# Optimization experiments

Hardware: AMD Instinct MI355X
Metric: run time of the kernel (lower is better)

The kernel has to match this reference:

```python
import jax, jax.numpy as jnp
import numpy as np

B, H, W, C = 2, 64, 64, 256
NH, K = 8, 7  # num_heads, neighborhood kernel size


def setup_inputs() -> dict:
    key = jax.random.key(0)
    ks = jax.random.split(key, 8)
    xav = lambda k, shape: jax.random.normal(k, shape, jnp.float32) * np.sqrt(2.0 / (shape[0] + shape[1])).astype(np.float32)
    return {
        "x": jax.random.normal(ks[0], (B, H, W, C), jnp.float32),
        "norm1_g": jnp.ones((C,), jnp.float32),
        "norm1_b": jnp.zeros((C,), jnp.float32),
        "qkv_w": xav(ks[1], (3 * C, C)),
        "qkv_b": jnp.zeros((3 * C,), jnp.float32),
        "rpb": jax.random.normal(ks[2], (NH, 2 * K - 1, 2 * K - 1), jnp.float32) * 0.02,
        "proj_w": xav(ks[3], (C, C)),
        "proj_b": jnp.zeros((C,), jnp.float32),
        "norm2_g": jnp.ones((C,), jnp.float32),
        "norm2_b": jnp.zeros((C,), jnp.float32),
        "fc1_w": xav(ks[4], (4 * C, C)),
        "fc1_b": jnp.zeros((4 * C,), jnp.float32),
        "fc2_w": xav(ks[5], (C, 4 * C)),
        "fc2_b": jnp.zeros((C,), jnp.float32),
    }


def _layernorm(x, g, b, eps=1e-5):
    m = x.mean(-1, keepdims=True)
    v = jnp.mean((x - m) ** 2, axis=-1, keepdims=True)
    return (x - m) * jax.lax.rsqrt(v + eps) * g + b


def _nat2d(x, qkv_w, qkv_b, rpb, proj_w, proj_b):
    """Neighborhood attention 2D (NATTEN semantics: edge-clamped k x k windows,
    relative positional bias indexed by key_pos - query_pos + k - 1)."""
    b, h, w, c = x.shape
    nh = rpb.shape[0]
    k = (rpb.shape[1] + 1) // 2
    dh = c // nh
    qkv = (x @ qkv_w.T + qkv_b).reshape(b, h, w, 3, nh, dh)
    q = qkv[..., 0, :, :] * (dh ** -0.5)  # [b,h,w,nh,dh]
    kk = qkv[..., 1, :, :]
    vv = qkv[..., 2, :, :]
    # edge-clamped window starts per query row/col
    starts_h = jnp.clip(jnp.arange(h) - k // 2, 0, h - k)
    starts_w = jnp.clip(jnp.arange(w) - k // 2, 0, w - k)
    idx_h = starts_h[:, None] + jnp.arange(k)  # [h,k] key row indices
    idx_w = starts_w[:, None] + jnp.arange(k)  # [w,k] key col indices
    # gather neighborhoods -> [b,h,w,k,k,nh,dh]
    knb = kk[:, idx_h][:, :, :, idx_w].transpose(0, 1, 3, 2, 4, 5, 6)
    vnb = vv[:, idx_h][:, :, :, idx_w].transpose(0, 1, 3, 2, 4, 5, 6)
    attn = jnp.einsum('bijhd,bijklhd->bijhkl', q, knb)  # [b,h,w,nh,k,k]
    # relative positional bias: index = key - query + (k-1) in [0, 2k-2]
    rb_h = idx_h - jnp.arange(h)[:, None] + (k - 1)  # [h,k]
    rb_w = idx_w - jnp.arange(w)[:, None] + (k - 1)  # [w,k]
    bias = rpb[:, rb_h][:, :, :, rb_w]  # [nh,h,k,w,k]
    bias = bias.transpose(1, 3, 0, 2, 4)  # [h,w,nh,k,k]
    attn = jax.nn.softmax((attn + bias).reshape(b, h, w, nh, k * k), axis=-1)
    out = jnp.einsum('bijhn,bijnhd->bijhd', attn, vnb.reshape(b, h, w, k * k, nh, dh))
    return out.reshape(b, h, w, c) @ proj_w.T + proj_b


def reference(x, norm1_g, norm1_b, qkv_w, qkv_b, rpb, proj_w, proj_b,
              norm2_g, norm2_b, fc1_w, fc1_b, fc2_w, fc2_b):
    # norm -> neighborhood attention -> residual
    x = x + _nat2d(_layernorm(x, norm1_g, norm1_b), qkv_w, qkv_b, rpb, proj_w, proj_b)
    # norm -> MLP (gelu) -> residual
    hdn = _layernorm(x, norm2_g, norm2_b)
    hdn = jax.nn.gelu(hdn @ fc1_w.T + fc1_b, approximate=False)
    return x + (hdn @ fc2_w.T + fc2_b)
```

## Files before the change

kernel.cpp:

```cpp
#include <hip/hip_runtime.h>

typedef __attribute__((ext_vector_type(8))) short bf16x8;
typedef __attribute__((ext_vector_type(4))) float f32x4;
typedef unsigned short u16;

__device__ __forceinline__ float bf2f(u16 u) {
    return __builtin_bit_cast(float, ((unsigned int)u) << 16);
}
__device__ __forceinline__ u16 f2bf(float f) {
    unsigned int x = __builtin_bit_cast(unsigned int, f);
    x += 0x7FFFu + ((x >> 16) & 1u);
    return (u16)(x >> 16);
}

typedef const __attribute__((address_space(1))) void* gas_t;
typedef __attribute__((address_space(3))) void* las_t;
__device__ __forceinline__ void load_lds16(const u16* g, u16* l) {
    __builtin_amdgcn_global_load_lds((gas_t)g, (las_t)l, 16, 0, 0);
}

__global__ __launch_bounds__(256) void cvt_kernel(
    const float* __restrict__ s0, const float* __restrict__ s1,
    const float* __restrict__ s2, const float* __restrict__ s3,
    u16* __restrict__ dst)
{
    const int i4 = (blockIdx.x * 256 + threadIdx.x) * 4;
    const float* src;
    int off;
    if      (i4 < 196608) { src = s0; off = i4; }
    else if (i4 < 262144) { src = s1; off = i4 - 196608; }
    else if (i4 < 524288) { src = s2; off = i4 - 262144; }
    else                  { src = s3; off = i4 - 524288; }
    float4 v = *(const float4*)(src + off);
    ushort4 o;
    o.x = f2bf(v.x); o.y = f2bf(v.y); o.z = f2bf(v.z); o.w = f2bf(v.w);
    *(ushort4*)(dst + i4) = o;
}

__global__ __launch_bounds__(256) void ln_kernel(
    const float* __restrict__ x, const float* __restrict__ g,
    const float* __restrict__ b, u16* __restrict__ y)
{
    const int tok  = blockIdx.x * 4 + (threadIdx.x >> 6);
    const int lane = threadIdx.x & 63;
    float4 v = *(const float4*)(x + (size_t)tok * 256 + lane * 4);
    float s  = v.x + v.y + v.z + v.w;
    float sq = v.x*v.x + v.y*v.y + v.z*v.z + v.w*v.w;
    #pragma unroll
    for (int off = 32; off; off >>= 1) {
        s  += __shfl_xor(s, off);
        sq += __shfl_xor(sq, off);
    }
    float mean = s * (1.0f / 256.0f);
    float var  = sq * (1.0f / 256.0f) - mean * mean;
    float rs   = rsqrtf(var + 1e-5f);
    float4 gv = *(const float4*)(g + lane * 4);
    float4 bv = *(const float4*)(b + lane * 4);
    ushort4 o;
    o.x = f2bf((v.x - mean) * rs * gv.x + bv.x);
    o.y = f2bf((v.y - mean) * rs * gv.y + bv.y);
    o.z = f2bf((v.z - mean) * rs * gv.z + bv.z);
    o.w = f2bf((v.w - mean) * rs * gv.w + bv.w);
    *(ushort4*)(y + (size_t)tok * 256 + lane * 4) = o;
}

template<int N, int K, int EPI>
__global__ __launch_bounds__(256) void gemm64(
    const u16* __restrict__ A, const u16* __restrict__ W,
    const float* __restrict__ bias, const float* __restrict__ res,
    void* __restrict__ outv)
{
    __shared__ u16 As[64 * 64];
    __shared__ u16 Bs[64 * 64];
    const int tid  = threadIdx.x;
    const int lane = tid & 63;
    const int wave = tid >> 6;
    const int m0   = blockIdx.x * 64;
    const int n0   = blockIdx.y * 64;
    const int wm0  = (wave >> 1) * 32;
    const int wn0  = (wave & 1) * 32;

    f32x4 acc[2][2];
    #pragma unroll
    for (int mt = 0; mt < 2; ++mt)
        #pragma unroll
        for (int nt = 0; nt < 2; ++nt)
            acc[mt][nt] = (f32x4){0.f, 0.f, 0.f, 0.f};

    int soff[2];
    #pragma unroll
    for (int r = 0; r < 2; ++r) {
        const int s   = r * 256 + tid;
        const int row = s >> 3;
        const int c   = (s & 7) ^ (row & 7);
        soff[r] = row * K + c * 8;
    }
    const int fr = lane & 15;
    const int fc = lane >> 4;

    for (int k0 = 0; k0 < K; k0 += 64) {
        __syncthreads();
        #pragma unroll
        for (int r = 0; r < 2; ++r) {
            load_lds16(A + (size_t)m0 * K + k0 + soff[r], As + (r * 256 + tid) * 8);
            load_lds16(W + (size_t)n0 * K + k0 + soff[r], Bs + (r * 256 + tid) * 8);
        }
        __syncthreads();
        #pragma unroll
        for (int ks = 0; ks < 2; ++ks) {
            bf16x8 af[2], bw[2];
            #pragma unroll
            for (int mt = 0; mt < 2; ++mt) {
                const int rr   = wm0 + mt * 16 + fr;
                const int phys = (ks * 4 + fc) ^ (rr & 7);
                af[mt] = *(const bf16x8*)(As + rr * 64 + phys * 8);
            }
            #pragma unroll
            for (int nt = 0; nt < 2; ++nt) {
                const int rr   = wn0 + nt * 16 + fr;
                const int phys = (ks * 4 + fc) ^ (rr & 7);
                bw[nt] = *(const bf16x8*)(Bs + rr * 64 + phys * 8);
            }
            #pragma unroll
            for (int mt = 0; mt < 2; ++mt)
                #pragma unroll
                for (int nt = 0; nt < 2; ++nt)
                    acc[mt][nt] = __builtin_amdgcn_mfma_f32_16x16x32_bf16(af[mt], bw[nt], acc[mt][nt], 0, 0, 0);
        }
    }

    const int col = lane & 15;
    const int rb  = (lane >> 4) * 4;
    #pragma unroll
    for (int nt = 0; nt < 2; ++nt) {
        const int n  = n0 + wn0 + nt * 16 + col;
        const float bv = bias[n];
        #pragma unroll
        for (int mt = 0; mt < 2; ++mt) {
            #pragma unroll
            for (int r = 0; r < 4; ++r) {
                const int m = m0 + wm0 + mt * 16 + rb + r;
                float v = acc[mt][nt][r] + bv;
                if (EPI == 1) {
                    if (n < 256) v *= 0.1767766952966369f;
                    ((u16*)outv)[(size_t)m * N + n] = f2bf(v);
                }
                if (EPI == 2) {
                    v += res[(size_t)m * N + n];
                    ((float*)outv)[(size_t)m * N + n] = v;
                }
                if (EPI == 3) {
                    v = 0.5f * v * (1.0f + erff(v * 0.7071067811865475f));
                    ((u16*)outv)[(size_t)m * N + n] = f2bf(v);
                }
            }
        }
    }
}

__global__ __launch_bounds__(256, 2) void attn_tile_kernel(
    const u16* __restrict__ qkv, const float* __restrict__ rpb,
    u16* __restrict__ out)
{
    __shared__ u16   kv[100 * 64];
    __shared__ u16   qs[16 * 32];
    __shared__ float probs[16 * 66];

    const int tid  = threadIdx.x;
    const int bb   = blockIdx.x >> 8;
    const int rem  = blockIdx.x & 255;
    const int ti0  = (rem >> 4) << 2;
    const int tj0  = (rem & 15) << 2;
    const int oh   = min(max(ti0 - 3, 0), 54);
    const int ow   = min(max(tj0 - 3, 0), 54);
    const int tokbase = bb * 4096;

    int off_kv[4];
    #pragma unroll
    for (int r = 0; r < 4; ++r) {
        const int s  = r * 256 + tid;
        const int t  = s >> 3;
        const int cs = s & 7;
        const int c  = cs ^ (t & 7);
        const int tr = t / 10, tc = t - tr * 10;
        const int tokg = tokbase + (oh + tr) * 64 + (ow + tc);
        off_kv[r] = tokg * 768 + 256 + ((c & 4) << 6) + (c & 3) * 8;
    }
    const int tq   = tid >> 2;
    const int qoff = (tokbase + (ti0 + (tq >> 2)) * 64 + (tj0 + (tq & 3))) * 768
                   + (tid & 3) * 8;

    const int token = tid >> 4;
    const int part  = tid & 15;
    const int li = token >> 2, lj = token & 3;
    const int i  = ti0 + li,   j  = tj0 + lj;
    const int sh = min(max(i - 3, 0), 57);
    const int sw = min(max(j - 3, 0), 57);
    const int rowbase  = (sh - oh) * 10 + (sw - ow);
    const int rb_const = (sh - i + 6) * 13 + (sw - j + 6);
    const size_t outbase = (size_t)(tokbase + i * 64 + j) * 256 + part * 2;

    for (int h = 0; h < 8; ++h) {
        __syncthreads();
        const int hoff = h * 32;
        #pragma unroll
        for (int r = 0; r < 3; ++r)
            load_lds16(qkv + off_kv[r] + hoff, kv + (r * 256 + tid) * 8);
        if (tid < 32)
            load_lds16(qkv + off_kv[3] + hoff, kv + (768 + tid) * 8);
        if (tid < 64)
            load_lds16(qkv + qoff + hoff, qs + tid * 8);
        __syncthreads();

        float qv[32];
        #pragma unroll
        for (int c = 0; c < 4; ++c) {
            bf16x8 v = *(const bf16x8*)(qs + token * 32 + c * 8);
            #pragma unroll
            for (int e = 0; e < 8; ++e) qv[c * 8 + e] = bf2f((u16)v[e]);
        }

        float sc[4];
        #pragma unroll
        for (int sidx = 0; sidx < 4; ++sidx) {
            const int n = part + sidx * 16;
            if (n < 49) {
                const int kh = n / 7, kw = n - (n / 7) * 7;
                const int hidx = rowbase + kh * 10 + kw;
                float acc = rpb[h * 169 + rb_const + kh * 13 + kw];
                #pragma unroll
                for (int c = 0; c < 4; ++c) {
                    const int slot = (hidx << 3) + (c ^ (hidx & 7));
                    bf16x8 kk = *(const bf16x8*)(kv + slot * 8);
                    #pragma unroll
                    for (int e = 0; e < 8; ++e)
                        acc += qv[c * 8 + e] * bf2f((u16)kk[e]);
                }
                sc[sidx] = acc;
            } else {
                sc[sidx] = -1e30f;
            }
        }
        float mx = fmaxf(fmaxf(sc[0], sc[1]), fmaxf(sc[2], sc[3]));
        #pragma unroll
        for (int off = 1; off < 16; off <<= 1) mx = fmaxf(mx, __shfl_xor(mx, off));
        float ex[4], ssum = 0.f;
        #pragma unroll
        for (int sidx = 0; sidx < 4; ++sidx) {
            ex[sidx] = __expf(sc[sidx] - mx);
            ssum += ex[sidx];
        }
        #pragma unroll
        for (int off = 1; off < 16; off <<= 1) ssum += __shfl_xor(ssum, off);
        const float inv = 1.0f / ssum;
        #pragma unroll
        for (int sidx = 0; sidx < 4; ++sidx)
            probs[token * 66 + part + sidx * 16] = ex[sidx] * inv;
        __syncthreads();

        float o0 = 0.f, o1 = 0.f;
        const int vchunk = 4 + (part >> 2);
        const int vsub   = (part & 3) * 2;
        #pragma unroll
        for (int kh = 0; kh < 7; ++kh) {
            #pragma unroll
            for (int kw = 0; kw < 7; ++kw) {
                const int n    = kh * 7 + kw;
                const int hidx = rowbase + kh * 10 + kw;
                const float p  = probs[token * 66 + n];
                const int slot = (hidx << 3) + (vchunk ^ (hidx & 7));
                const unsigned int vv = *(const unsigned int*)(kv + slot * 8 + vsub);
                o0 += p * bf2f((u16)(vv & 0xffffu));
                o1 += p * bf2f((u16)(vv >> 16));
            }
        }
        ushort2 ov;
        ov.x = f2bf(o0); ov.y = f2bf(o1);
        *(ushort2*)(out + outbase + hoff) = ov;
    }
}

extern "C" void kernel_launch(void* const* d_in, const int* in_sizes, int n_in,
                              void* d_out, int out_size, void* d_ws, size_t ws_size,
                              hipStream_t stream)
{
    const float* x      = (const float*)d_in[0];
    const float* n1g    = (const float*)d_in[1];
    const float* n1b    = (const float*)d_in[2];
    const float* qkv_w  = (const float*)d_in[3];
    const float* qkv_b  = (const float*)d_in[4];
    const float* rpb    = (const float*)d_in[5];
    const float* proj_w = (const float*)d_in[6];
    const float* proj_b = (const float*)d_in[7];
    const float* n2g    = (const float*)d_in[8];
    const float* n2b    = (const float*)d_in[9];
    const float* fc1_w  = (const float*)d_in[10];
    const float* fc1_b  = (const float*)d_in[11];
    const float* fc2_w  = (const float*)d_in[12];
    const float* fc2_b  = (const float*)d_in[13];
    float* out = (float*)d_out;

    char* wsb = (char*)d_ws;
    u16*   wbf   = (u16*)wsb;
    u16*   qkvW  = wbf;
    u16*   projW = wbf + 196608;
    u16*   fc1W  = wbf + 262144;
    u16*   fc2W  = wbf + 524288;
    u16*   ln1   = (u16*)(wsb + 1572864);
    u16*   attn  = ln1;
    u16*   qkvB  = (u16*)(wsb + 5767168);
    u16*   ln2   = qkvB;
    u16*   hbuf  = (u16*)(wsb + 9961472);
    float* x1    = (float*)(wsb + 26738688);

    dim3 blk(256);
    cvt_kernel<<<768, blk, 0, stream>>>(qkv_w, proj_w, fc1_w, fc2_w, wbf);
    ln_kernel<<<2048, blk, 0, stream>>>(x, n1g, n1b, ln1);
    gemm64<768, 256, 1><<<dim3(128, 12), blk, 0, stream>>>(ln1, qkvW, qkv_b, nullptr, qkvB);
    attn_tile_kernel<<<512, blk, 0, stream>>>(qkvB, rpb, attn);
    gemm64<256, 256, 2><<<dim3(128, 4), blk, 0, stream>>>(attn, projW, proj_b, x, x1);
    ln_kernel<<<2048, blk, 0, stream>>>(x1, n2g, n2b, ln2);
    gemm64<1024, 256, 3><<<dim3(128, 16), blk, 0, stream>>>(ln2, fc1W, fc1_b, nullptr, hbuf);
    gemm64<256, 1024, 2><<<dim3(128, 4), blk, 0, stream>>>(hbuf, fc2W, fc2_b, x1, out);
}
```

Baseline: 165.1 us.

## Fuse whole block into persistent megakernel with grid barriers; fuse proj with LayerNorm2

```diff
diff --git a/kernel.cpp b/kernel.cpp
--- a/kernel.cpp
+++ b/kernel.cpp
@@ -3,6 +3,8 @@
 typedef __attribute__((ext_vector_type(8))) short bf16x8;
 typedef __attribute__((ext_vector_type(4))) float f32x4;
 typedef unsigned short u16;
+
+#define NBLK 512
 
 __device__ __forceinline__ float bf2f(u16 u) {
     return __builtin_bit_cast(float, ((unsigned int)u) << 16);
@@ -19,64 +21,33 @@
     __builtin_amdgcn_global_load_lds((gas_t)g, (las_t)l, 16, 0, 0);
 }
 
-__global__ __launch_bounds__(256) void cvt_kernel(
-    const float* __restrict__ s0, const float* __restrict__ s1,
-    const float* __restrict__ s2, const float* __restrict__ s3,
-    u16* __restrict__ dst)
+__global__ void init_bar(int* bar) {
+    if (threadIdx.x < 16) bar[threadIdx.x] = 0;
+}
+
+__device__ __forceinline__ void gridbar(int* bar, int idx) {
+    __syncthreads();
+    if (threadIdx.x == 0) {
+        __threadfence();
+        __hip_atomic_fetch_add(bar + idx, 1, __ATOMIC_ACQ_REL, __HIP_MEMORY_SCOPE_AGENT);
+        while (__hip_atomic_load(bar + idx, __ATOMIC_ACQUIRE, __HIP_MEMORY_SCOPE_AGENT) < NBLK)
+            __builtin_amdgcn_s_sleep(8);
+    }
+    __syncthreads();
+    __threadfence();
+}
+
+template<int N, int K, int EPI>
+__device__ void gemm_tile(int bx, int by, const u16* A, const u16* W,
+                          const float* bias, const float* res, void* outv, char* smem)
 {
-    const int i4 = (blockIdx.x * 256 + threadIdx.x) * 4;
-    const float* src;
-    int off;
-    if      (i4 < 196608) { src = s0; off = i4; }
-    else if (i4 < 262144) { src = s1; off = i4 - 196608; }
-    else if (i4 < 524288) { src = s2; off = i4 - 262144; }
-    else                  { src = s3; off = i4 - 524288; }
-    float4 v = *(const float4*)(src + off);
-    ushort4 o;
-    o.x = f2bf(v.x); o.y = f2bf(v.y); o.z = f2bf(v.z); o.w = f2bf(v.w);
-    *(ushort4*)(dst + i4) = o;
-}
-
-__global__ __launch_bounds__(256) void ln_kernel(
-    const float* __restrict__ x, const float* __restrict__ g,
-    const float* __restrict__ b, u16* __restrict__ y)
-{
-    const int tok  = blockIdx.x * 4 + (threadIdx.x >> 6);
-    const int lane = threadIdx.x & 63;
-    float4 v = *(const float4*)(x + (size_t)tok * 256 + lane * 4);
-    float s  = v.x + v.y + v.z + v.w;
-    float sq = v.x*v.x + v.y*v.y + v.z*v.z + v.w*v.w;
-    #pragma unroll
-    for (int off = 32; off; off >>= 1) {
-        s  += __shfl_xor(s, off);
-        sq += __shfl_xor(sq, off);
-    }
-    float mean = s * (1.0f / 256.0f);
-    float var  = sq * (1.0f / 256.0f) - mean * mean;
-    float rs   = rsqrtf(var + 1e-5f);
-    float4 gv = *(const float4*)(g + lane * 4);
-    float4 bv = *(const float4*)(b + lane * 4);
-    ushort4 o;
-    o.x = f2bf((v.x - mean) * rs * gv.x + bv.x);
-    o.y = f2bf((v.y - mean) * rs * gv.y + bv.y);
-    o.z = f2bf((v.z - mean) * rs * gv.z + bv.z);
-    o.w = f2bf((v.w - mean) * rs * gv.w + bv.w);
-    *(ushort4*)(y + (size_t)tok * 256 + lane * 4) = o;
-}
-
-template<int N, int K, int EPI>
-__global__ __launch_bounds__(256) void gemm64(
-    const u16* __restrict__ A, const u16* __restrict__ W,
-    const float* __restrict__ bias, const float* __restrict__ res,
-    void* __restrict__ outv)
-{
-    __shared__ u16 As[64 * 64];
-    __shared__ u16 Bs[64 * 64];
+    u16* As = (u16*)smem;
+    u16* Bs = (u16*)(smem + 8192);
     const int tid  = threadIdx.x;
     const int lane = tid & 63;
     const int wave = tid >> 6;
-    const int m0   = blockIdx.x * 64;
-    const int n0   = blockIdx.y * 64;
+    const int m0   = bx * 64;
+    const int n0   = by * 64;
     const int wm0  = (wave >> 1) * 32;
     const int wn0  = (wave & 1) * 32;
 
@@ -158,17 +129,106 @@
     }
 }
 
-__global__ __launch_bounds__(256, 2) void attn_tile_kernel(
-    const u16* __restrict__ qkv, const float* __restrict__ rpb,
-    u16* __restrict__ out)
+__device__ void proj_ln_tile(int bx, const u16* A, const u16* W, const float* pb,
+                             const float* xres, const float* g2, const float* b2,
+                             float* x1, u16* ln2out, char* smem)
 {
-    __shared__ u16   kv[100 * 64];
-    __shared__ u16   qs[16 * 32];
-    __shared__ float probs[16 * 66];
-
+    u16* As = (u16*)smem;
+    u16* Bs = (u16*)(smem + 4096);
     const int tid  = threadIdx.x;
-    const int bb   = blockIdx.x >> 8;
-    const int rem  = blockIdx.x & 255;
+    const int lane = tid & 63;
+    const int wave = tid >> 6;
+    const int m0   = bx * 64;
+
+    f32x4 acc[16];
+    #pragma unroll
+    for (int nt = 0; nt < 16; ++nt) acc[nt] = (f32x4){0.f, 0.f, 0.f, 0.f};
+
+    const int arow = tid >> 2, acs = tid & 3;
+    const int aoff = (m0 + arow) * 256 + (acs ^ (arow & 3)) * 8;
+    int boff[4];
+    #pragma unroll
+    for (int r = 0; r < 4; ++r) {
+        const int s   = r * 256 + tid;
+        const int row = s >> 2;
+        const int c   = (s & 3) ^ (row & 3);
+        boff[r] = row * 256 + c * 8;
+    }
+    const int fr = lane & 15;
+    const int fc = lane >> 4;
+
+    for (int k0 = 0; k0 < 256; k0 += 32) {
+        __syncthreads();
+        load_lds16(A + aoff + k0, As + tid * 8);
+        #pragma unroll
+        for (int r = 0; r < 4; ++r)
+            load_lds16(W + boff[r] + k0, Bs + (r * 256 + tid) * 8);
+        __syncthreads();
+        const int ra   = wave * 16 + fr;
+        const int pa   = fc ^ (ra & 3);
+        bf16x8 af = *(const bf16x8*)(As + ra * 32 + pa * 8);
+        #pragma unroll
+        for (int nt = 0; nt < 16; ++nt) {
+            const int rb_  = nt * 16 + fr;
+            const int pb_  = fc ^ (rb_ & 3);
+            bf16x8 bw = *(const bf16x8*)(Bs + rb_ * 32 + pb_ * 8);
+            acc[nt] = __builtin_amdgcn_mfma_f32_16x16x32_bf16(af, bw, acc[nt], 0, 0, 0);
+        }
+    }
+
+    const int col = lane & 15;
+    const int g   = lane >> 4;
+    float s[4] = {0.f, 0.f, 0.f, 0.f}, sq[4] = {0.f, 0.f, 0.f, 0.f};
+    #pragma unroll
+    for (int nt = 0; nt < 16; ++nt) {
+        const int n = nt * 16 + col;
+        const float bv = pb[n];
+        #pragma unroll
+        for (int r = 0; r < 4; ++r) {
+            const int m = m0 + wave * 16 + g * 4 + r;
+            float v = acc[nt][r] + bv + xres[(size_t)m * 256 + n];
+            acc[nt][r] = v;
+            s[r] += v; sq[r] += v * v;
+        }
+    }
+    #pragma unroll
+    for (int off = 1; off < 16; off <<= 1) {
+        #pragma unroll
+        for (int r = 0; r < 4; ++r) {
+            s[r]  += __shfl_xor(s[r], off);
+            sq[r] += __shfl_xor(sq[r], off);
+        }
+    }
+    float mean[4], rs[4];
+    #pragma unroll
+    for (int r = 0; r < 4; ++r) {
+        mean[r] = s[r] * (1.0f / 256.0f);
+        const float var = sq[r] * (1.0f / 256.0f) - mean[r] * mean[r];
+        rs[r] = rsqrtf(var + 1e-5f);
+    }
+    #pragma unroll
+    for (int nt = 0; nt < 16; ++nt) {
+        const int n = nt * 16 + col;
+        const float gam = g2[n], bet = b2[n];
+        #pragma unroll
+        for (int r = 0; r < 4; ++r) {
+            const int m = m0 + wave * 16 + g * 4 + r;
+            const float v = acc[nt][r];
+            x1[(size_t)m * 256 + n] = v;
+            ln2out[(size_t)m * 256 + n] = f2bf((v - mean[r]) * rs[r] * gam + bet);
+        }
+    }
+}
+
+__device__ void attn_tile(int bid, const u16* qkv, const float* rpb, u16* out, char* smem)
+{
+    u16*   kv    = (u16*)smem;
+    u16*   qs    = (u16*)(smem + 12800);
+    float* probs = (float*)(smem + 13824);
+
+    const int tid  = threadIdx.x;
+    const int bb   = bid >> 8;
+    const int rem  = bid & 255;
     const int ti0  = (rem >> 4) << 2;
     const int tj0  = (rem & 15) << 2;
     const int oh   = min(max(ti0 - 3, 0), 54);
@@ -178,10 +238,9 @@
     int off_kv[4];
     #pragma unroll
     for (int r = 0; r < 4; ++r) {
-        const int s  = r * 256 + tid;
-        const int t  = s >> 3;
-        const int cs = s & 7;
-        const int c  = cs ^ (t & 7);
+        const int sslot = r * 256 + tid;
+        const int t  = sslot >> 3;
+        const int c  = (sslot & 7) ^ (t & 7);
         const int tr = t / 10, tc = t - tr * 10;
         const int tokg = tokbase + (oh + tr) * 64 + (ow + tc);
         off_kv[r] = tokg * 768 + 256 + ((c & 4) << 6) + (c & 3) * 8;
@@ -278,6 +337,89 @@
         ov.x = f2bf(o0); ov.y = f2bf(o1);
         *(ushort2*)(out + outbase + hoff) = ov;
     }
+}
+
+__global__ __launch_bounds__(256, 2) void mega_kernel(
+    const float* __restrict__ x,
+    const float* __restrict__ n1g, const float* __restrict__ n1b,
+    const float* __restrict__ qkv_w, const float* __restrict__ qkv_b,
+    const float* __restrict__ rpb,
+    const float* __restrict__ proj_w, const float* __restrict__ proj_b,
+    const float* __restrict__ n2g, const float* __restrict__ n2b,
+    const float* __restrict__ fc1_w, const float* __restrict__ fc1_b,
+    const float* __restrict__ fc2_w, const float* __restrict__ fc2_b,
+    float* __restrict__ out, char* __restrict__ wsb, int* __restrict__ bar)
+{
+    __shared__ __align__(16) char smem[20608];
+    const int bid = blockIdx.x;
+    const int tid = threadIdx.x;
+
+    u16* wbf   = (u16*)wsb;
+    u16* qkvW  = wbf;
+    u16* projW = wbf + 196608;
+    u16* fc1W  = wbf + 262144;
+    u16* fc2W  = wbf + 524288;
+    u16*   ln1   = (u16*)(wsb + (2u  << 20));
+    u16*   qkvB  = (u16*)(wsb + (6u  << 20));
+    u16*   attnB = (u16*)(wsb + (20u << 20));
+    u16*   ln2   = (u16*)(wsb + (24u << 20));
+    u16*   hbuf  = (u16*)(wsb + (28u << 20));
+    float* x1    = (float*)(wsb + (44u << 20));
+
+    {
+        #pragma unroll
+        for (int r = 0; r < 6; ++r) {
+            const int idx = bid * 256 + tid + r * 131072;
+            const float* src; int off;
+            if      (idx < 196608) { src = qkv_w;  off = idx; }
+            else if (idx < 262144) { src = proj_w; off = idx - 196608; }
+            else if (idx < 524288) { src = fc1_w;  off = idx - 262144; }
+            else                   { src = fc2_w;  off = idx - 524288; }
+            wbf[idx] = f2bf(src[off]);
+        }
+        const int wave = tid >> 6, lane = tid & 63;
+        #pragma unroll
+        for (int it = 0; it < 4; ++it) {
+            const int tok = bid * 16 + it * 4 + wave;
+            float4 v = *(const float4*)(x + (size_t)tok * 256 + lane * 4);
+            float s  = v.x + v.y + v.z + v.w;
+            float sq = v.x*v.x + v.y*v.y + v.z*v.z + v.w*v.w;
+            #pragma unroll
+            for (int off = 32; off; off >>= 1) {
+                s  += __shfl_xor(s, off);
+                sq += __shfl_xor(sq, off);
+            }
+            const float mean = s * (1.0f / 256.0f);
+            const float var  = sq * (1.0f / 256.0f) - mean * mean;
+            const float rs   = rsqrtf(var + 1e-5f);
+            float4 gv = *(const float4*)(n1g + lane * 4);
+            float4 bv = *(const float4*)(n1b + lane * 4);
+            ushort4 o;
+            o.x = f2bf((v.x - mean) * rs * gv.x + bv.x);
+            o.y = f2bf((v.y - mean) * rs * gv.y + bv.y);
+            o.z = f2bf((v.z - mean) * rs * gv.z + bv.z);
+            o.w = f2bf((v.w - mean) * rs * gv.w + bv.w);
+            *(ushort4*)(ln1 + (size_t)tok * 256 + lane * 4) = o;
+        }
+    }
+    gridbar(bar, 0);
+
+    for (int t = bid; t < 1536; t += NBLK)
+        gemm_tile<768, 256, 1>(t & 127, t >> 7, ln1, qkvW, qkv_b, nullptr, qkvB, smem);
+    gridbar(bar, 1);
+
+    attn_tile(bid, qkvB, rpb, attnB, smem);
+    gridbar(bar, 2);
+
+    if (bid < 128)
+        proj_ln_tile(bid, attnB, projW, proj_b, x, n2g, n2b, x1, ln2, smem);
+    gridbar(bar, 3);
+
+    for (int t = bid; t < 2048; t += NBLK)
+        gemm_tile<1024, 256, 3>(t & 127, t >> 7, ln2, fc1W, fc1_b, nullptr, hbuf, smem);
+    gridbar(bar, 4);
+
+    gemm_tile<256, 1024, 2>(bid & 127, bid >> 7, hbuf, fc2W, fc2_b, x1, out, smem);
 }
 
 extern "C" void kernel_launch(void* const* d_in, const int* in_sizes, int n_in,
@@ -301,25 +443,10 @@
     float* out = (float*)d_out;
 
     char* wsb = (char*)d_ws;
-    u16*   wbf   = (u16*)wsb;
-    u16*   qkvW  = wbf;
-    u16*   projW = wbf + 196608;
-    u16*   fc1W  = wbf + 262144;
-    u16*   fc2W  = wbf + 524288;
-    u16*   ln1   = (u16*)(wsb + 1572864);
-    u16*   attn  = ln1;
-    u16*   qkvB  = (u16*)(wsb + 5767168);
-    u16*   ln2   = qkvB;
-    u16*   hbuf  = (u16*)(wsb + 9961472);
-    float* x1    = (float*)(wsb + 26738688);
-
-    dim3 blk(256);
-    cvt_kernel<<<768, blk, 0, stream>>>(qkv_w, proj_w, fc1_w, fc2_w, wbf);
-    ln_kernel<<<2048, blk, 0, stream>>>(x, n1g, n1b, ln1);
-    gemm64<768, 256, 1><<<dim3(128, 12), blk, 0, stream>>>(ln1, qkvW, qkv_b, nullptr, qkvB);
-    attn_tile_kernel<<<512, blk, 0, stream>>>(qkvB, rpb, attn);
-    gemm64<256, 256, 2><<<dim3(128, 4), blk, 0, stream>>>(attn, projW, proj_b, x, x1);
-    ln_kernel<<<2048, blk, 0, stream>>>(x1, n2g, n2b, ln2);
-    gemm64<1024, 256, 3><<<dim3(128, 16), blk, 0, stream>>>(ln2, fc1W, fc1_b, nullptr, hbuf);
-    gemm64<256, 1024, 2><<<dim3(128, 4), blk, 0, stream>>>(hbuf, fc2W, fc2_b, x1, out);
-}
+    int*  bar = (int*)(wsb + (64u << 20));
+
+    init_bar<<<1, 64, 0, stream>>>(bar);
+    mega_kernel<<<NBLK, 256, 0, stream>>>(
+        x, n1g, n1b, qkv_w, qkv_b, rpb, proj_w, proj_b,
+        n2g, n2b, fc1_w, fc1_b, fc2_w, fc2_b, out, wsb, bar);
+}
```

New measurement: 623.9 us. 278% more time.
